# Performance work log

Hardware: AMD Instinct MI355X
Metric: run time of the kernel (lower is better)

## Reference

```python
import jax, jax.numpy as jnp
import numpy as np

B, S, D = 1, 4096, 896
NH, NKV, HD = 14, 2, 64
ROPE_BASE = 1000000.0

def rotate_half(x):
    x1, x2 = x[..., :x.shape[-1] // 2], x[..., x.shape[-1] // 2:]
    return jnp.concatenate((-x2, x1), axis=-1)

def rope_tables(seq_len, head_dim, base):
    inv_freq = 1.0 / (base ** (jnp.arange(0, head_dim, 2, dtype=jnp.float32) / head_dim))
    t = jnp.arange(seq_len, dtype=jnp.float32)
    freqs = jnp.einsum('i,j->ij', t, inv_freq)
    emb = jnp.concatenate((freqs, freqs), axis=-1)  # [S, HD]
    return jnp.cos(emb), jnp.sin(emb)

def setup_inputs() -> dict:
    key = jax.random.key(0)
    ks = jax.random.split(key, 6)
    hidden_states = jax.random.normal(ks[0], (B, S, D), dtype=jnp.float32)
    # additive causal mask [1,1,S,S]
    neg = jnp.finfo(jnp.float32).min
    causal = jnp.where(jnp.tril(jnp.ones((S, S), dtype=bool)), 0.0, neg)
    attention_mask = causal[None, None, :, :].astype(jnp.float32)
    sc = 0.02
    Wq = jax.random.normal(ks[1], (D, NH * HD), dtype=jnp.float32) * sc
    Wk = jax.random.normal(ks[2], (D, NKV * HD), dtype=jnp.float32) * sc
    Wv = jax.random.normal(ks[3], (D, NKV * HD), dtype=jnp.float32) * sc
    Wo = jax.random.normal(ks[4], (D, D), dtype=jnp.float32) * sc
    bq = jnp.zeros((NH * HD,), jnp.float32)
    bk = jnp.zeros((NKV * HD,), jnp.float32)
    bv = jnp.zeros((NKV * HD,), jnp.float32)
    return {"hidden_states": hidden_states, "attention_mask": attention_mask,
            "Wq": Wq, "bq": bq, "Wk": Wk, "bk": bk, "Wv": Wv, "bv": bv, "Wo": Wo}

def reference(hidden_states, attention_mask, Wq, bq, Wk, bk, Wv, bv, Wo):
    b, s, _ = hidden_states.shape
    groups = NH // NKV
    q = (hidden_states @ Wq + bq).reshape(b, s, NH, HD)
    k = (hidden_states @ Wk + bk).reshape(b, s, NKV, HD)
    v = (hidden_states @ Wv + bv).reshape(b, s, NKV, HD)
    cos, sin = rope_tables(s, HD, ROPE_BASE)
    cos = cos[None, :, None, :]
    sin = sin[None, :, None, :]
    q = q * cos + rotate_half(q) * sin
    k = k * cos + rotate_half(k) * sin
    # GQA: repeat KV heads
    k = jnp.repeat(k, groups, axis=2)
    v = jnp.repeat(v, groups, axis=2)
    # [b, h, s, d]
    q = jnp.transpose(q, (0, 2, 1, 3))
    k = jnp.transpose(k, (0, 2, 1, 3))
    v = jnp.transpose(v, (0, 2, 1, 3))
    attn = jnp.einsum('bhqd,bhkd->bhqk', q, k) / jnp.sqrt(jnp.float32(HD))
    attn = attn + attention_mask
    attn = jax.nn.softmax(attn, axis=-1)
    out = jnp.einsum('bhqk,bhkd->bhqd', attn, v)
    out = jnp.transpose(out, (0, 2, 1, 3)).reshape(b, s, NH * HD)
    return out @ Wo
```

## Files before the change

### kernel.cpp

```cpp
#include <hip/hip_runtime.h>
#include <math.h>

constexpr int S_    = 4096;
constexpr int Dm    = 896;
constexpr int NHd   = 14;
constexpr int NKVh  = 2;
constexpr int HDim  = 64;
constexpr int NQ    = NHd * HDim;
constexpr int NK    = NKVh * HDim;
constexpr int NQK   = NQ + NK;
constexpr int GROUPS = NHd / NKVh;
constexpr float L2B   = 19.9315685693241740873f;
constexpr float LOG2E = 1.44269504088896340736f;

constexpr int NUNITS = 952;

typedef __attribute__((ext_vector_type(8)))  short bf16x8;
typedef __attribute__((ext_vector_type(4)))  short bf16x4;
typedef __attribute__((ext_vector_type(4)))  float f32x4;
typedef __attribute__((ext_vector_type(16))) float f32x16;
typedef __attribute__((ext_vector_type(4)))  int   i32x4;

__device__ __forceinline__ short f2bf(float f) {
  unsigned u = __builtin_bit_cast(unsigned, f);
  unsigned r = (u + 0x7FFFu + ((u >> 16) & 1u)) >> 16;
  return (short)r;
}
__device__ __forceinline__ float bf2f(short s) {
  return __builtin_bit_cast(float, ((unsigned)(unsigned short)s) << 16);
}

__device__ __forceinline__ unsigned cvtpk(float lo, float hi) {
  unsigned r;
  asm("v_cvt_pk_bf16_f32 %0, %1, %2" : "=v"(r) : "v"(lo), "v"(hi));
  return r;
}

__device__ __forceinline__ void gload16(const void* g, void* l) {
  __builtin_amdgcn_global_load_lds(
      (const __attribute__((address_space(1))) unsigned int*)g,
      (__attribute__((address_space(3))) unsigned int*)l, 16, 0, 0);
}

__global__ __launch_bounds__(256) void prep_small(
    const float* __restrict__ hs, short* __restrict__ hsb,
    float* __restrict__ cost, float* __restrict__ sint)
{
  int bid = blockIdx.x;
  if (bid < 1792) {
    int idx = bid * 256 + threadIdx.x;
    float4 a = ((const float4*)hs)[idx * 2];
    float4 b = ((const float4*)hs)[idx * 2 + 1];
    bf16x8 o;
    o[0] = f2bf(a.x); o[1] = f2bf(a.y); o[2] = f2bf(a.z); o[3] = f2bf(a.w);
    o[4] = f2bf(b.x); o[5] = f2bf(b.y); o[6] = f2bf(b.z); o[7] = f2bf(b.w);
    ((bf16x8*)hsb)[idx] = o;
  } else {
    int idx = (bid - 1792) * 256 + threadIdx.x;
    int m = idx >> 5, j = idx & 31;
    float invf = exp2f(-(float)j * (L2B / 32.0f));
    float th = (float)m * invf;
    float s, c;
    sincosf(th, &s, &c);
    cost[idx] = c;
    sint[idx] = s;
  }
}

__global__ __launch_bounds__(256) void transpose_all(
    const float* __restrict__ Wq, const float* __restrict__ Wk,
    const float* __restrict__ Wv, const float* __restrict__ Wo,
    short* __restrict__ wtq, short* __restrict__ wto)
{
  __shared__ float t[64 * 68];
  const int kt = blockIdx.x;
  const int by = blockIdx.y;
  const int tid = threadIdx.x;

  const float* src; int srcN, nt; short* dst; int rowOff;
  if (by < 14)      { src = Wq; srcN = NQ; nt = by;      dst = wtq; rowOff = 0; }
  else if (by < 16) { src = Wk; srcN = NK; nt = by - 14; dst = wtq; rowOff = 896; }
  else if (by < 18) { src = Wv; srcN = NK; nt = by - 16; dst = wtq; rowOff = 1024; }
  else              { src = Wo; srcN = NQ; nt = by - 18; dst = wto; rowOff = 0; }

  #pragma unroll
  for (int i = 0; i < 4; i++) {
    int idx = tid + i * 256;
    int r = idx >> 4, c4 = (idx & 15) * 4;
    *(float4*)&t[r * 68 + c4] =
        *(const float4*)&src[(size_t)(kt * 64 + r) * srcN + nt * 64 + c4];
  }
  __syncthreads();
  const int nl = tid >> 2;
  const int kc = (tid & 3) * 16;
  bf16x8 o0, o1;
  #pragma unroll
  for (int i = 0; i < 8; i++) o0[i] = f2bf(t[(kc + i) * 68 + nl]);
  #pragma unroll
  for (int i = 0; i < 8; i++) o1[i] = f2bf(t[(kc + 8 + i) * 68 + nl]);
  short* dp = dst + (size_t)(rowOff + nt * 64 + nl) * 896 + kt * 64 + kc;
  *(bf16x8*)dp = o0;
  *(bf16x8*)(dp + 8) = o1;
}

template<int EPI>
__global__ __launch_bounds__(256) void gemm64(
    const short* __restrict__ A, const short* __restrict__ Bt,
    const float* __restrict__ biasq, const float* __restrict__ biask,
    const float* __restrict__ biasv,
    const float* __restrict__ cost, const float* __restrict__ sint,
    short* __restrict__ qkb, short* __restrict__ vtb,
    float* __restrict__ outp)
{
  __shared__ short Als[64 * 64];
  __shared__ short Bls[128 * 64];
  const int tid = threadIdx.x;
  const int lane = tid & 63;
  const int w = tid >> 6;
  const int wm = w >> 1, wn = w & 1;
  const int r16 = lane & 15, rg = lane >> 4;
  const int bm = blockIdx.x, bn = blockIdx.y;

  const f32x4 zero4 = {0.f, 0.f, 0.f, 0.f};
  f32x4 acc[2][4];
  #pragma unroll
  for (int mt = 0; mt < 2; mt++)
    #pragma unroll
    for (int nt = 0; nt < 4; nt++) acc[mt][nt] = zero4;

  const int srow = (lane >> 3);
  const int scol = (lane & 7) * 8;

  for (int kt = 0; kt < 14; ++kt) {
    __syncthreads();
    #pragma unroll
    for (int i = 0; i < 2; i++) {
      int c = w * 2 + i;
      int row = c * 8 + srow;
      gload16(A + (size_t)(bm * 64 + row) * 896 + kt * 64 + scol, &Als[c * 512]);
    }
    #pragma unroll
    for (int i = 0; i < 4; i++) {
      int c = w * 4 + i;
      int row = c * 8 + srow;
      gload16(Bt + (size_t)(bn * 128 + row) * 896 + kt * 64 + scol, &Bls[c * 512]);
    }
    __syncthreads();

    bf16x8 af[2][2], bfr[4][2];
    #pragma unroll
    for (int mt = 0; mt < 2; mt++)
      #pragma unroll
      for (int ks = 0; ks < 2; ks++)
        af[mt][ks] = *(const bf16x8*)&Als[(wm * 32 + mt * 16 + r16) * 64 + ks * 32 + rg * 8];
    #pragma unroll
    for (int nt = 0; nt < 4; nt++)
      #pragma unroll
      for (int ks = 0; ks < 2; ks++)
        bfr[nt][ks] = *(const bf16x8*)&Bls[(wn * 64 + nt * 16 + r16) * 64 + ks * 32 + rg * 8];
    #pragma unroll
    for (int mt = 0; mt < 2; mt++)
      #pragma unroll
      for (int nt = 0; nt < 4; nt++)
        #pragma unroll
        for (int ks = 0; ks < 2; ks++)
          acc[mt][nt] = __builtin_amdgcn_mfma_f32_16x16x32_bf16(
              af[mt][ks], bfr[nt][ks], acc[mt][nt], 0, 0, 0);
  }

  if (EPI == 0) {
    const int nbase = bn * 128 + wn * 64;
    if (bn < 8) {
      const float scl = (bn < 7) ? (0.125f * LOG2E) : 1.0f;
      const float* bias = (bn < 7) ? biasq : (biask - 896);
      #pragma unroll
      for (int mt = 0; mt < 2; mt++) {
        const int m0 = bm * 64 + wm * 32 + mt * 16 + rg * 4;
        #pragma unroll
        for (int nt = 0; nt < 4; nt++) {
          int n = nbase + nt * 16 + r16;
          int j = n & 31;
          float sgn = (n & 32) ? 1.f : -1.f;
          float b0 = bias[n], b1 = bias[n ^ 32];
          #pragma unroll
          for (int r = 0; r < 4; r++) {
            int m = m0 + r;
            float c_ = cost[m * 32 + j], s_ = sint[m * 32 + j];
            float val = ((acc[mt][nt][r] + b0) * c_ +
                         sgn * (acc[mt][nt ^ 2][r] + b1) * s_) * scl;
            qkb[(size_t)m * NQK + n] = f2bf(val);
          }
        }
      }
    } else {
      #pragma unroll
      for (int mt = 0; mt < 2; mt++) {
        const int m0 = bm * 64 + wm * 32 + mt * 16 + rg * 4;
        #pragma unroll
        for (int nt = 0; nt < 4; nt++) {
          int vc = wn * 64 + nt * 16 + r16;
          float b0 = biasv[vc];
          bf16x4 pk;
          #pragma unroll
          for (int r = 0; r < 4; r++) pk[r] = f2bf(acc[mt][nt][r] + b0);
          *(bf16x4*)&vtb[(size_t)vc * S_ + m0] = pk;
        }
      }
    }
  } else {
    #pragma unroll
    for (int mt = 0; mt < 2; mt++) {
      const int m0 = bm * 64 + wm * 32 + mt * 16 + rg * 4;
      #pragma unroll
      for (int nt = 0; nt < 4; nt++) {
        int n = bn * 128 + wn * 64 + nt * 16 + r16;
        #pragma unroll
        for (int r = 0; r < 4; r++)
          outp[(size_t)(m0 + r) * NQ + n] = acc[mt][nt][r];
      }
    }
  }
}

__global__ __launch_bounds__(256, 3) void flash_mfma(
    const short* __restrict__ qkb, const short* __restrict__ vtb,
    short* __restrict__ attnb, short* __restrict__ orec,
    float* __restrict__ mlrec, unsigned* __restrict__ cnt)
{
  __shared__ __align__(16) char lds[32768];
  __shared__ int s_unit;

  const int tid  = threadIdx.x;
  const int lane = tid & 63;
  const int w    = tid >> 6;
  const int q32  = lane & 31;
  const int hi   = lane >> 5;

  const int c8   = tid & 7;
  const int key0 = tid >> 3;
  const int key1 = key0 + 32;
  const int swz0 = (c8 ^ (key0 & 7)) << 4;
  const int swz1 = (c8 ^ (key1 & 7)) << 4;

  bf16x8 ones;
  #pragma unroll
  for (int j = 0; j < 8; j++) ones[j] = (short)0x3F80;

  for (;;) {
    __syncthreads();
    if (tid == 0) s_unit = (int)atomicAdd(cnt, 1u);
    __syncthreads();
    const int u = s_unit;
    if (u >= NUNITS) break;

    const int e = u / 14;
    const int h = u - e * 14;
    int qt, ci;
    if (e < 36)      { qt = 31 - e / 3; ci = e - (31 - qt) * 3; }
    else if (e < 60) { int f = e - 36; qt = 19 - (f >> 1); ci = f & 1; }
    else             { qt = 67 - e; ci = 0; }
    const int K  = 2 * (qt + 1);
    const int n  = (qt < 8) ? 1 : (qt < 20) ? 2 : 3;
    const int L  = (K + n - 1) / n;
    const int kt_lo = ci * L;
    const int kt_hi = (kt_lo + L < K) ? (kt_lo + L) : K;
    const int kv = h / GROUPS;
    const int q0 = qt * 128;
    const int kbase2 = (NQ + kv * HDim) * 2;
    const int qg = q0 + w * 32 + q32;

    bf16x8 qf[4];
    {
      const short* qp = qkb + (size_t)qg * NQK + h * HDim + hi * 8;
      #pragma unroll
      for (int ks = 0; ks < 4; ++ks) qf[ks] = *(const bf16x8*)(qp + ks * 16);
    }

    f32x16 acc_o[2], acc_l;
    float m_run = 0.f;
    #pragma unroll
    for (int r = 0; r < 16; ++r) { acc_o[0][r] = 0.f; acc_o[1][r] = 0.f; acc_l[r] = 0.f; }

    const char* ksrc0 = (const char*)qkb + (size_t)(kt_lo * 64 + key0) * 2048 + kbase2 + swz0;
    const char* ksrc1 = (const char*)qkb + (size_t)(kt_lo * 64 + key1) * 2048 + kbase2 + swz1;
    const char* vsrc0 = (const char*)vtb + (size_t)(kv * 64 + key0) * 8192 + (size_t)kt_lo * 128 + swz0;
    const char* vsrc1 = (const char*)vtb + (size_t)(kv * 64 + key1) * 8192 + (size_t)kt_lo * 128 + swz1;

    gload16(ksrc0, lds + w * 1024);
    gload16(ksrc1, lds + 4096 + w * 1024);
    gload16(vsrc0, lds + 8192 + w * 1024);
    gload16(vsrc1, lds + 12288 + w * 1024);
    ksrc0 += 131072; ksrc1 += 131072;
    vsrc0 += 128;    vsrc1 += 128;

    for (int kt = kt_lo; kt < kt_hi; ++kt) {
      const int cur = (kt - kt_lo) & 1;
      asm volatile("s_waitcnt vmcnt(0)" ::: "memory");
      __builtin_amdgcn_s_barrier();
      if (kt + 1 < kt_hi) {
        char* B = lds + ((cur ^ 1) << 14);
        gload16(ksrc0, B + w * 1024);
        gload16(ksrc1, B + 4096 + w * 1024);
        gload16(vsrc0, B + 8192 + w * 1024);
        gload16(vsrc1, B + 12288 + w * 1024);
        ksrc0 += 131072; ksrc1 += 131072;
        vsrc0 += 128;    vsrc1 += 128;
      }
      __builtin_amdgcn_sched_barrier(0);
      const char* KsB = lds + (cur << 14);
      const char* VtB = KsB + 8192;
      const int kb = kt * 64;

      f32x16 sc[2];
      #pragma unroll
      for (int r = 0; r < 16; ++r) { sc[0][r] = 0.f; sc[1][r] = 0.f; }
      #pragma unroll
      for (int t = 0; t < 2; ++t) {
        const int key = t * 32 + q32;
        #pragma unroll
        for (int ks = 0; ks < 4; ++ks) {
          bf16x8 kf = *(const bf16x8*)(KsB + key * 128 + (((2 * ks + hi) ^ (key & 7)) << 4));
          sc[t] = __builtin_amdgcn_mfma_f32_32x32x16_bf16(kf, qf[ks], sc[t], 0, 0, 0);
        }
      }

      if (kb + 63 > q0 + w * 32) {
        #pragma unroll
        for (int t = 0; t < 2; ++t)
          #pragma unroll
          for (int r = 0; r < 16; ++r) {
            int key = kb + t * 32 + (r & 3) + 8 * (r >> 2) + 4 * hi;
            sc[t][r] = (key > qg) ? -1e30f : sc[t][r];
          }
      }

      f32x16 mm;
      #pragma unroll
      for (int r = 0; r < 16; ++r) mm[r] = fmaxf(sc[0][r], sc[1][r]);
      #pragma unroll
      for (int r = 0; r < 8; ++r) mm[r] = fmaxf(mm[r], mm[r + 8]);
      #pragma unroll
      for (int r = 0; r < 4; ++r) mm[r] = fmaxf(mm[r], mm[r + 4]);
      float pm = fmaxf(fmaxf(mm[0], mm[1]), fmaxf(mm[2], mm[3]));
      {
        float a = pm, b = pm;
        asm("v_permlane32_swap_b32 %0, %1" : "+v"(a), "+v"(b));
        pm = fmaxf(a, b);
      }

      if (!__all(pm <= m_run + 8.0f)) {
        float newm = fmaxf(m_run, pm);
        float scl = exp2f(m_run - newm);
        m_run = newm;
        acc_l[0] *= scl;
        #pragma unroll
        for (int r = 0; r < 16; ++r) { acc_o[0][r] *= scl; acc_o[1][r] *= scl; }
      }

      #pragma unroll
      for (int t = 0; t < 2; ++t)
        #pragma unroll
        for (int r = 0; r < 16; ++r) sc[t][r] = exp2f(sc[t][r] - m_run);

      unsigned U0[2][4], U1[2][4];
      #pragma unroll
      for (int t = 0; t < 2; ++t)
        #pragma unroll
        for (int a = 0; a < 4; ++a) {
          U0[t][a] = cvtpk(sc[t][4 * a],     sc[t][4 * a + 1]);
          U1[t][a] = cvtpk(sc[t][4 * a + 2], sc[t][4 * a + 3]);
        }

      #pragma unroll
      for (int kp = 0; kp < 4; ++kp) {
        const int t = kp >> 1, c = kp & 1;
        unsigned x0 = U0[t][2 * c], y0 = U0[t][2 * c + 1];
        unsigned x1 = U1[t][2 * c], y1 = U1[t][2 * c + 1];
        asm("v_permlane32_swap_b32 %0, %1" : "+v"(x0), "+v"(y0));
        asm("v_permlane32_swap_b32 %0, %1" : "+v"(x1), "+v"(y1));
        i32x4 pi = {(int)x0, (int)x1, (int)y0, (int)y1};
        bf16x8 pf = __builtin_bit_cast(bf16x8, pi);
        acc_l = __builtin_amdgcn_mfma_f32_32x32x16_bf16(ones, pf, acc_l, 0, 0, 0);
        #pragma unroll
        for (int dt = 0; dt < 2; ++dt) {
          const int d = dt * 32 + q32;
          bf16x8 vf = *(const bf16x8*)(VtB + d * 128 + (((2 * kp + hi) ^ (d & 7)) << 4));
          acc_o[dt] = __builtin_amdgcn_mfma_f32_32x32x16_bf16(vf, pf, acc_o[dt], 0, 0, 0);
        }
      }
    }

    if (n == 1) {
      const float inv = 1.0f / acc_l[0];
      short* op = attnb + (size_t)qg * NQ + h * HDim + 4 * hi;
      #pragma unroll
      for (int dt = 0; dt < 2; ++dt)
        #pragma unroll
        for (int rq = 0; rq < 4; ++rq) {
          bf16x4 pk;
          pk[0] = f2bf(acc_o[dt][4 * rq]     * inv);
          pk[1] = f2bf(acc_o[dt][4 * rq + 1] * inv);
          pk[2] = f2bf(acc_o[dt][4 * rq + 2] * inv);
          pk[3] = f2bf(acc_o[dt][4 * rq + 3] * inv);
          *(bf16x4*)(op + dt * 32 + 8 * rq) = pk;
        }
    } else {
      const int qloc = w * 32 + q32;
      short* op;
      if (ci == 0) {
        op = attnb + (size_t)qg * NQ + h * HDim + 4 * hi;
      } else {
        int er = (qt < 20) ? (h * 36 + (qt - 8))
                           : (h * 36 + 12 + (qt - 20) * 2 + (ci - 1));
        op = orec + (size_t)er * 8192 + (size_t)qloc * 64 + 4 * hi;
      }
      #pragma unroll
      for (int dt = 0; dt < 2; ++dt)
        #pragma unroll
        for (int rq = 0; rq < 4; ++rq) {
          bf16x4 pk;
          pk[0] = f2bf(acc_o[dt][4 * rq]);
          pk[1] = f2bf(acc_o[dt][4 * rq + 1]);
          pk[2] = f2bf(acc_o[dt][4 * rq + 2]);
          pk[3] = f2bf(acc_o[dt][4 * rq + 3]);
          *(bf16x4*)(op + dt * 32 + 8 * rq) = pk;
        }
      if (hi == 0) {
        int co = (qt < 20) ? (8 + (qt - 8) * 2 + ci) : (32 + (qt - 20) * 3 + ci);
        float2 ml = {m_run, acc_l[0]};
        *(float2*)(mlrec + ((size_t)(h * 68 + co) * 128 + qloc) * 2) = ml;
      }
    }
  }
}

__global__ __launch_bounds__(128) void merge_chunks(
    const short* __restrict__ orec, const float* __restrict__ mlrec,
    short* __restrict__ attnb)
{
  const int b = blockIdx.x;
  const int h = b / 24;
  const int qt = 8 + (b - h * 24);
  const int n = (qt < 20) ? 2 : 3;
  const int qloc = threadIdx.x;
  const int q = qt * 128 + qloc;

  const int co0 = (qt < 20) ? (8 + (qt - 8) * 2) : (32 + (qt - 20) * 3);
  float2 ml0 = *(const float2*)(mlrec + ((size_t)(h * 68 + co0)     * 128 + qloc) * 2);
  float2 ml1 = *(const float2*)(mlrec + ((size_t)(h * 68 + co0 + 1) * 128 + qloc) * 2);
  float2 ml2 = (n == 3)
      ? *(const float2*)(mlrec + ((size_t)(h * 68 + co0 + 2) * 128 + qloc) * 2)
      : float2{-3.0e38f, 0.f};

  float M = fmaxf(fmaxf(ml0.x, ml1.x), ml2.x);
  float a0 = exp2f(ml0.x - M), a1 = exp2f(ml1.x - M);
  float a2 = (n == 3) ? exp2f(ml2.x - M) : 0.f;
  float inv = 1.0f / (a0 * ml0.y + a1 * ml1.y + a2 * ml2.y);
  float s0 = a0 * inv, s1 = a1 * inv, s2 = a2 * inv;

  const int er1 = (qt < 20) ? (h * 36 + (qt - 8)) : (h * 36 + 12 + (qt - 20) * 2);
  short* O0 = attnb + (size_t)q * NQ + h * HDim;
  const short* O1 = orec + (size_t)er1 * 8192 + (size_t)qloc * 64;
  const short* O2 = (n == 3) ? (O1 + 8192) : O1;

  #pragma unroll
  for (int i = 0; i < 8; i++) {
    bf16x8 x0 = *(const bf16x8*)(O0 + i * 8);
    bf16x8 x1 = *(const bf16x8*)(O1 + i * 8);
    bf16x8 x2 = *(const bf16x8*)(O2 + i * 8);
    bf16x8 o;
    #pragma unroll
    for (int j = 0; j < 8; j++)
      o[j] = f2bf(s0 * bf2f(x0[j]) + s1 * bf2f(x1[j]) + s2 * bf2f(x2[j]));
    *(bf16x8*)(O0 + i * 8) = o;
  }
}

extern "C" void kernel_launch(void* const* d_in, const int* in_sizes, int n_in,
                              void* d_out, int out_size, void* d_ws, size_t ws_size,
                              hipStream_t stream)
{
  const float* hs = (const float*)d_in[0];
  const float* Wq = (const float*)d_in[2];
  const float* bq = (const float*)d_in[3];
  const float* Wk = (const float*)d_in[4];
  const float* bk = (const float*)d_in[5];
  const float* Wv = (const float*)d_in[6];
  const float* bv = (const float*)d_in[7];
  const float* Wo = (const float*)d_in[8];

  short* hsb  = (short*)d_ws;
  short* wtq  = hsb + (size_t)S_ * Dm;
  short* wto  = wtq + (size_t)1152 * 896;
  float* cost = (float*)(wto + (size_t)896 * 896);
  float* sint = cost + (size_t)S_ * 32;
  short* qkb  = (short*)(sint + (size_t)S_ * 32);
  short* vtb  = qkb + (size_t)S_ * NQK;
  short* attnb= vtb + (size_t)NK * S_;
  float* out  = (float*)d_out;

  short*    orec  = hsb;
  float*    mlrec = cost;
  unsigned* cnt   = (unsigned*)((char*)attnb + (size_t)S_ * NQ * 2);

  hipLaunchKernelGGL(prep_small, dim3(2304), dim3(256), 0, stream, hs, hsb, cost, sint);
  hipLaunchKernelGGL(transpose_all, dim3(14, 32), dim3(256), 0, stream,
                     Wq, Wk, Wv, Wo, wtq, wto);
  hipLaunchKernelGGL((gemm64<0>), dim3(64, 9), dim3(256), 0, stream,
                     hsb, wtq, bq, bk, bv, cost, sint, qkb, vtb, (float*)nullptr);
  hipMemsetAsync(cnt, 0, 4, stream);
  hipLaunchKernelGGL(flash_mfma, dim3(768), dim3(256), 0, stream,
                     qkb, vtb, attnb, orec, mlrec, cnt);
  hipLaunchKernelGGL(merge_chunks, dim3(336), dim3(128), 0, stream,
                     orec, mlrec, attnb);
  hipLaunchKernelGGL((gemm64<1>), dim3(64, 7), dim3(256), 0, stream,
                     attnb, wto, bq, bk, bv, cost, sint,
                     (short*)nullptr, (short*)nullptr, out);
}
```

Baseline: 133.6 us.

## Triple-buffer K/V tiles in flash attention and merge prep kernels

```diff
diff --git a/kernel.cpp b/kernel.cpp
--- a/kernel.cpp
+++ b/kernel.cpp
@@ -42,21 +42,27 @@
       (__attribute__((address_space(3))) unsigned int*)l, 16, 0, 0);
 }
 
-__global__ __launch_bounds__(256) void prep_small(
+__global__ __launch_bounds__(256) void prep_all(
     const float* __restrict__ hs, short* __restrict__ hsb,
-    float* __restrict__ cost, float* __restrict__ sint)
+    float* __restrict__ cost, float* __restrict__ sint,
+    const float* __restrict__ Wq, const float* __restrict__ Wk,
+    const float* __restrict__ Wv, const float* __restrict__ Wo,
+    short* __restrict__ wtq, short* __restrict__ wto)
 {
-  int bid = blockIdx.x;
+  const int bid = blockIdx.x;
+  const int tid = threadIdx.x;
   if (bid < 1792) {
-    int idx = bid * 256 + threadIdx.x;
+    int idx = bid * 256 + tid;
     float4 a = ((const float4*)hs)[idx * 2];
     float4 b = ((const float4*)hs)[idx * 2 + 1];
     bf16x8 o;
     o[0] = f2bf(a.x); o[1] = f2bf(a.y); o[2] = f2bf(a.z); o[3] = f2bf(a.w);
     o[4] = f2bf(b.x); o[5] = f2bf(b.y); o[6] = f2bf(b.z); o[7] = f2bf(b.w);
     ((bf16x8*)hsb)[idx] = o;
-  } else {
-    int idx = (bid - 1792) * 256 + threadIdx.x;
+    return;
+  }
+  if (bid < 2304) {
+    int idx = (bid - 1792) * 256 + tid;
     int m = idx >> 5, j = idx & 31;
     float invf = exp2f(-(float)j * (L2B / 32.0f));
     float th = (float)m * invf;
@@ -64,18 +70,12 @@
     sincosf(th, &s, &c);
     cost[idx] = c;
     sint[idx] = s;
-  }
-}
-
-__global__ __launch_bounds__(256) void transpose_all(
-    const float* __restrict__ Wq, const float* __restrict__ Wk,
-    const float* __restrict__ Wv, const float* __restrict__ Wo,
-    short* __restrict__ wtq, short* __restrict__ wto)
-{
+    return;
+  }
   __shared__ float t[64 * 68];
-  const int kt = blockIdx.x;
-  const int by = blockIdx.y;
-  const int tid = threadIdx.x;
+  const int b2 = bid - 2304;
+  const int kt = b2 % 14;
+  const int by = b2 / 14;
 
   const float* src; int srcN, nt; short* dst; int rowOff;
   if (by < 14)      { src = Wq; srcN = NQ; nt = by;      dst = wtq; rowOff = 0; }
@@ -227,7 +227,7 @@
     short* __restrict__ attnb, short* __restrict__ orec,
     float* __restrict__ mlrec, unsigned* __restrict__ cnt)
 {
-  __shared__ __align__(16) char lds[32768];
+  __shared__ __align__(16) char lds[49152];
   __shared__ int s_unit;
 
   const int tid  = threadIdx.x;
@@ -292,13 +292,27 @@
     gload16(vsrc1, lds + 12288 + w * 1024);
     ksrc0 += 131072; ksrc1 += 131072;
     vsrc0 += 128;    vsrc1 += 128;
-
+    if (kt_lo + 1 < kt_hi) {
+      char* B = lds + 16384;
+      gload16(ksrc0, B + w * 1024);
+      gload16(ksrc1, B + 4096 + w * 1024);
+      gload16(vsrc0, B + 8192 + w * 1024);
+      gload16(vsrc1, B + 12288 + w * 1024);
+      ksrc0 += 131072; ksrc1 += 131072;
+      vsrc0 += 128;    vsrc1 += 128;
+    }
+
+    int cur = 0;
     for (int kt = kt_lo; kt < kt_hi; ++kt) {
-      const int cur = (kt - kt_lo) & 1;
-      asm volatile("s_waitcnt vmcnt(0)" ::: "memory");
+      if (kt + 1 < kt_hi) {
+        asm volatile("s_waitcnt vmcnt(4)" ::: "memory");
+      } else {
+        asm volatile("s_waitcnt vmcnt(0)" ::: "memory");
+      }
       __builtin_amdgcn_s_barrier();
-      if (kt + 1 < kt_hi) {
-        char* B = lds + ((cur ^ 1) << 14);
+      if (kt + 2 < kt_hi) {
+        int nb = cur + 2; if (nb >= 3) nb -= 3;
+        char* B = lds + (nb << 14);
         gload16(ksrc0, B + w * 1024);
         gload16(ksrc1, B + 4096 + w * 1024);
         gload16(vsrc0, B + 8192 + w * 1024);
@@ -388,6 +402,7 @@
           acc_o[dt] = __builtin_amdgcn_mfma_f32_32x32x16_bf16(vf, pf, acc_o[dt], 0, 0, 0);
         }
       }
+      cur = (cur == 2) ? 0 : cur + 1;
     }
 
     if (n == 1) {
@@ -503,9 +518,8 @@
   float*    mlrec = cost;
   unsigned* cnt   = (unsigned*)((char*)attnb + (size_t)S_ * NQ * 2);
 
-  hipLaunchKernelGGL(prep_small, dim3(2304), dim3(256), 0, stream, hs, hsb, cost, sint);
-  hipLaunchKernelGGL(transpose_all, dim3(14, 32), dim3(256), 0, stream,
-                     Wq, Wk, Wv, Wo, wtq, wto);
+  hipLaunchKernelGGL(prep_all, dim3(2752), dim3(256), 0, stream,
+                     hs, hsb, cost, sint, Wq, Wk, Wv, Wo, wtq, wto);
   hipLaunchKernelGGL((gemm64<0>), dim3(64, 9), dim3(256), 0, stream,
                      hsb, wtq, bq, bk, bv, cost, sint, qkb, vtb, (float*)nullptr);
   hipMemsetAsync(cnt, 0, 4, stream);
```

After: 130.8 us. 2.1% less time.
